# Kernel tuning notes

Measured on AMD Instinct MI355X. Metric: run time of the kernel, lower is better.

The kernel has to match this reference:

```python
import jax, jax.numpy as jnp
import numpy as np

N = 50000        # nodes
E = 800000       # edges (avg degree 16)
D_IN = 128
HID = 128
K = 3


def cheb_edge_weights(row, col, n):
    # PyG ChebConv sym normalization with assumed lambda_max = 2.0:
    # L_hat = (2/lambda_max) * (I - D^-1/2 A D^-1/2) - I = -D^-1/2 A D^-1/2 (zero diagonal)
    mask = (row != col).astype(jnp.float32)  # remove_self_loops
    deg = jax.ops.segment_sum(mask, row, num_segments=n)
    dinv = jnp.where(deg > 0.0, jax.lax.rsqrt(jnp.maximum(deg, 1.0)), 0.0)
    return -dinv[row] * dinv[col] * mask  # [E]


def cheb_conv(x, row, col, w_edge, W, b, n):
    # Chebyshev recursion: Tx0=x, Tx1=L_hat x, Tx_k = 2 L_hat Tx_{k-1} - Tx_{k-2}
    def prop(h):  # sparse L_hat @ h via gather + segment_sum
        return jax.ops.segment_sum(w_edge[:, None] * h[col], row, num_segments=n)

    Tx0 = x
    out = Tx0 @ W[0]
    Tx1 = prop(Tx0)
    out = out + Tx1 @ W[1]
    for k in range(2, W.shape[0]):
        Tx2 = 2.0 * prop(Tx1) - Tx0
        out = out + Tx2 @ W[k]
        Tx0, Tx1 = Tx1, Tx2
    return out + b


def setup_inputs() -> dict:
    key = jax.random.key(0)
    ks = jax.random.split(key, 8)
    x = jax.random.normal(ks[0], (N, D_IN), dtype=jnp.float32)
    ei = jax.random.randint(ks[1], (2, E), 0, N, dtype=jnp.int32)
    s = 0.05
    W1 = jax.random.normal(ks[2], (K, D_IN, HID), dtype=jnp.float32) * s
    b1 = jnp.zeros((HID,), dtype=jnp.float32)
    W2 = jax.random.normal(ks[3], (K, HID, HID), dtype=jnp.float32) * s
    b2 = jnp.zeros((HID,), dtype=jnp.float32)
    W3 = jax.random.normal(ks[4], (K, HID, HID), dtype=jnp.float32) * s
    b3 = jnp.zeros((HID,), dtype=jnp.float32)
    return {"x": x, "ei": ei, "W1": W1, "b1": b1, "W2": W2, "b2": b2, "W3": W3, "b3": b3}


def reference(x, ei, W1, b1, W2, b2, W3, b3):
    row, col = ei[0], ei[1]
    w_edge = cheb_edge_weights(row, col, N)
    # layer chain: ChebConv -> ReLU -> dropout (eval mode: identity)
    h = jax.nn.relu(cheb_conv(x, row, col, w_edge, W1, b1, N))
    h = jax.nn.relu(cheb_conv(h, row, col, w_edge, W2, b2, N))
    h = jax.nn.relu(cheb_conv(h, row, col, w_edge, W3, b3, N))
    return h
```

## Files before the change

kernel.cpp:

```cpp
#include <hip/hip_runtime.h>
#include <hip/hip_bf16.h>

#define DFEAT 128

typedef short bf16x8 __attribute__((ext_vector_type(8)));
typedef float f32x4  __attribute__((ext_vector_type(4)));
typedef unsigned short u16x8 __attribute__((ext_vector_type(8)));

__device__ __forceinline__ unsigned bf16r(float f) {
    unsigned u = __float_as_uint(f);
    u += 0x7fffu + ((u >> 16) & 1u);
    return u >> 16;
}
__device__ __forceinline__ unsigned pack_bf16(float lo, float hi) {
    return bf16r(lo) | (bf16r(hi) << 16);
}

__global__ void deg_kernel(const int* __restrict__ ei, int* __restrict__ deg, int E) {
    int e = blockIdx.x * blockDim.x + threadIdx.x;
    if (e < E) {
        int r = ei[e];
        int c = ei[E + e];
        if (r != c) atomicAdd(&deg[r], 1);
    }
}

__global__ void dinv_kernel(const int* __restrict__ deg, float* __restrict__ dinv, int n) {
    int i = blockIdx.x * blockDim.x + threadIdx.x;
    if (i < n) {
        int d = deg[i];
        dinv[i] = (d > 0) ? rsqrtf((float)d) : 0.f;
    }
}

__global__ __launch_bounds__(1024) void scan1_kernel(const int* __restrict__ deg,
                                                     int* __restrict__ row_ptr,
                                                     int* __restrict__ bsum, int n) {
    __shared__ int wsums[16];
    int t = threadIdx.x;
    int idx = blockIdx.x * 1024 + t;
    int v = (idx < n) ? deg[idx] : 0;
    int vi = v;
    #pragma unroll
    for (int off = 1; off < 64; off <<= 1) {
        int x = __shfl_up(vi, off);
        if ((t & 63) >= off) vi += x;
    }
    if ((t & 63) == 63) wsums[t >> 6] = vi;
    __syncthreads();
    if (t < 16) {
        int s = wsums[t];
        int si = s;
        #pragma unroll
        for (int off = 1; off < 16; off <<= 1) {
            int x = __shfl_up(si, off);
            if (t >= off) si += x;
        }
        wsums[t] = si - s;
        if (t == 15) bsum[blockIdx.x] = si;
    }
    __syncthreads();
    if (idx < n) row_ptr[idx + 1] = wsums[t >> 6] + vi;
}

__global__ void scan2_kernel(int* __restrict__ bsum, int nb) {
    int t = threadIdx.x;
    int carry = 0;
    for (int base = 0; base < nb; base += 64) {
        int v = (base + t < nb) ? bsum[base + t] : 0;
        int vi = v;
        #pragma unroll
        for (int off = 1; off < 64; off <<= 1) {
            int x = __shfl_up(vi, off);
            if (t >= off) vi += x;
        }
        if (base + t < nb) bsum[base + t] = carry + vi - v;
        carry += __shfl(vi, 63);
    }
}

__global__ __launch_bounds__(1024) void scan3_kernel(int* __restrict__ row_ptr,
                                                     const int* __restrict__ bsum, int n) {
    int idx = blockIdx.x * 1024 + threadIdx.x;
    if (idx == 0) row_ptr[0] = 0;
    if (idx < n) row_ptr[idx + 1] += bsum[blockIdx.x];
}

__global__ void fill_kernel(const int* __restrict__ ei, const int* __restrict__ row_ptr,
                            int* __restrict__ fillc, const float* __restrict__ dinv,
                            int* __restrict__ e_col, float* __restrict__ e_w, int E) {
    int e = blockIdx.x * blockDim.x + threadIdx.x;
    if (e < E) {
        int r = ei[e];
        int c = ei[E + e];
        if (r != c) {
            int pos = row_ptr[r] + atomicAdd(&fillc[r], 1);
            e_col[pos] = c;
            e_w[pos] = -dinv[r] * dinv[c];
        }
    }
}

__global__ void xconv_kernel(const float2* __restrict__ x, unsigned* __restrict__ xb, int n2) {
    int id = blockIdx.x * blockDim.x + threadIdx.x;
    if (id < n2) {
        float2 v = x[id];
        xb[id] = pack_bf16(v.x, v.y);
    }
}

__global__ void wprep_kernel(const float* __restrict__ W1, const float* __restrict__ W2,
                             const float* __restrict__ W3, unsigned short* __restrict__ Wt) {
    int id = blockIdx.x * blockDim.x + threadIdx.x;
    const int PER = 3 * DFEAT * DFEAT;
    if (id < 3 * PER) {
        int layer = id / PER;
        int rem = id - layer * PER;
        const float* W = (layer == 0) ? W1 : ((layer == 1) ? W2 : W3);
        int seg = rem >> 14;
        int k   = (rem >> 7) & 127;
        int nn  = rem & 127;
        Wt[layer * PER + (seg << 14) + (nn << 7) + k] = (unsigned short)bf16r(W[rem]);
    }
}

__global__ __launch_bounds__(256) void prop_bf16_kernel(
    const unsigned* __restrict__ hin, const unsigned* __restrict__ sub,
    unsigned* __restrict__ hout,
    const int* __restrict__ row_ptr, const int* __restrict__ e_col,
    const float* __restrict__ e_w, float alpha, int n)
{
    int wv = __builtin_amdgcn_readfirstlane(threadIdx.x >> 6);
    int node = blockIdx.x * 4 + wv;
    int t = threadIdx.x & 63;
    if (node >= n) return;
    int s = row_ptr[node];
    int e = row_ptr[node + 1];
    float a0 = 0.f, a1 = 0.f;
    int j = s;
    for (; j + 8 <= e; j += 8) {
        int c0 = e_col[j+0], c1 = e_col[j+1], c2 = e_col[j+2], c3 = e_col[j+3];
        int c4 = e_col[j+4], c5 = e_col[j+5], c6 = e_col[j+6], c7 = e_col[j+7];
        float w0 = e_w[j+0], w1 = e_w[j+1], w2 = e_w[j+2], w3 = e_w[j+3];
        float w4 = e_w[j+4], w5 = e_w[j+5], w6 = e_w[j+6], w7 = e_w[j+7];
        unsigned v0 = hin[(size_t)c0 * 64 + t];
        unsigned v1 = hin[(size_t)c1 * 64 + t];
        unsigned v2 = hin[(size_t)c2 * 64 + t];
        unsigned v3 = hin[(size_t)c3 * 64 + t];
        unsigned v4 = hin[(size_t)c4 * 64 + t];
        unsigned v5 = hin[(size_t)c5 * 64 + t];
        unsigned v6 = hin[(size_t)c6 * 64 + t];
        unsigned v7 = hin[(size_t)c7 * 64 + t];
        a0 += w0 * __uint_as_float(v0 << 16);  a1 += w0 * __uint_as_float(v0 & 0xffff0000u);
        a0 += w1 * __uint_as_float(v1 << 16);  a1 += w1 * __uint_as_float(v1 & 0xffff0000u);
        a0 += w2 * __uint_as_float(v2 << 16);  a1 += w2 * __uint_as_float(v2 & 0xffff0000u);
        a0 += w3 * __uint_as_float(v3 << 16);  a1 += w3 * __uint_as_float(v3 & 0xffff0000u);
        a0 += w4 * __uint_as_float(v4 << 16);  a1 += w4 * __uint_as_float(v4 & 0xffff0000u);
        a0 += w5 * __uint_as_float(v5 << 16);  a1 += w5 * __uint_as_float(v5 & 0xffff0000u);
        a0 += w6 * __uint_as_float(v6 << 16);  a1 += w6 * __uint_as_float(v6 & 0xffff0000u);
        a0 += w7 * __uint_as_float(v7 << 16);  a1 += w7 * __uint_as_float(v7 & 0xffff0000u);
    }
    for (; j < e; ++j) {
        int c = e_col[j];
        float w = e_w[j];
        unsigned v = hin[(size_t)c * 64 + t];
        a0 += w * __uint_as_float(v << 16);
        a1 += w * __uint_as_float(v & 0xffff0000u);
    }
    a0 *= alpha; a1 *= alpha;
    if (sub) {
        unsigned v = sub[(size_t)node * 64 + t];
        a0 -= __uint_as_float(v << 16);
        a1 -= __uint_as_float(v & 0xffff0000u);
    }
    hout[(size_t)node * 64 + t] = pack_bf16(a0, a1);
}

#define WPAD 136
__global__ __launch_bounds__(256) void gemm3_mfma_kernel(
    const unsigned short* __restrict__ X0, const unsigned short* __restrict__ X1,
    const unsigned short* __restrict__ X2,
    const unsigned short* __restrict__ Wt, const float* __restrict__ bias,
    void* __restrict__ out, int n, int out_bf16)
{
    __shared__ unsigned short Ws[DFEAT * WPAD];
    const int t    = threadIdx.x;
    const int wave = t >> 6;
    const int lane = t & 63;
    const int quad = lane >> 4;
    const int l16  = lane & 15;

    const int row_base = blockIdx.x * 128 + wave * 32;
    int r0 = row_base + l16;       if (r0 >= n) r0 = n - 1;
    int r1 = row_base + 16 + l16;  if (r1 >= n) r1 = n - 1;

    const unsigned short* Xps[3] = {X0, X1, X2};

    f32x4 acc[2][8];
    #pragma unroll
    for (int tt = 0; tt < 2; ++tt)
        #pragma unroll
        for (int c = 0; c < 8; ++c) acc[tt][c] = (f32x4){0.f, 0.f, 0.f, 0.f};

    const int srow = t >> 1;
    const int shalf = (t & 1) * 64;

    #pragma unroll
    for (int seg = 0; seg < 3; ++seg) {
        __syncthreads();
        const unsigned short* Wp = Wt + (seg << 14);
        #pragma unroll
        for (int i = 0; i < 8; ++i) {
            *(u16x8*)&Ws[srow * WPAD + shalf + i * 8] =
                *(const u16x8*)&Wp[srow * DFEAT + shalf + i * 8];
        }
        __syncthreads();
        const unsigned short* A0 = Xps[seg] + (size_t)r0 * DFEAT;
        const unsigned short* A1 = Xps[seg] + (size_t)r1 * DFEAT;
        #pragma unroll
        for (int kk = 0; kk < 4; ++kk) {
            const int ko = kk * 32 + quad * 8;
            bf16x8 a0 = *(const bf16x8*)(A0 + ko);
            bf16x8 a1 = *(const bf16x8*)(A1 + ko);
            #pragma unroll
            for (int c = 0; c < 8; ++c) {
                bf16x8 b = *(const bf16x8*)&Ws[(c * 16 + l16) * WPAD + ko];
                acc[0][c] = __builtin_amdgcn_mfma_f32_16x16x32_bf16(a0, b, acc[0][c], 0, 0, 0);
                acc[1][c] = __builtin_amdgcn_mfma_f32_16x16x32_bf16(a1, b, acc[1][c], 0, 0, 0);
            }
        }
    }

    #pragma unroll
    for (int tt = 0; tt < 2; ++tt) {
        int orow0 = blockIdx.x * 128 + wave * 32 + tt * 16 + quad * 4;
        #pragma unroll
        for (int c = 0; c < 8; ++c) {
            int col = c * 16 + l16;
            float bv = bias[col];
            #pragma unroll
            for (int r = 0; r < 4; ++r) {
                int orow = orow0 + r;
                if (orow < n) {
                    float v = fmaxf(acc[tt][c][r] + bv, 0.f);
                    if (out_bf16)
                        ((unsigned short*)out)[(size_t)orow * DFEAT + col] = (unsigned short)bf16r(v);
                    else
                        ((float*)out)[(size_t)orow * DFEAT + col] = v;
                }
            }
        }
    }
}

extern "C" void kernel_launch(void* const* d_in, const int* in_sizes, int n_in,
                              void* d_out, int out_size, void* d_ws, size_t ws_size,
                              hipStream_t stream) {
    const float* x  = (const float*)d_in[0];
    const int*   ei = (const int*)d_in[1];
    const float* W1 = (const float*)d_in[2];
    const float* b1 = (const float*)d_in[3];
    const float* W2 = (const float*)d_in[4];
    const float* b2 = (const float*)d_in[5];
    const float* W3 = (const float*)d_in[6];
    const float* b3 = (const float*)d_in[7];

    const int N = in_sizes[0] / DFEAT;
    const int E = in_sizes[1] / 2;
    const int NPK = N * (DFEAT / 2);
    const int NB = (N + 1023) / 1024;

    unsigned* xb  = (unsigned*)d_ws;
    unsigned* t1b = xb  + NPK;
    unsigned* t2b = t1b + NPK;
    unsigned* ab  = t2b + NPK;
    unsigned short* wt = (unsigned short*)(ab + NPK);
    int*   deg     = (int*)(wt + 3 * 3 * DFEAT * DFEAT);
    int*   fillc   = deg + N;
    int*   row_ptr = fillc + N;
    float* dinv    = (float*)(row_ptr + (N + 1));
    int*   e_col   = (int*)(dinv + N);
    float* e_w     = (float*)(e_col + E);
    int*   bsum    = (int*)(e_w + E);

    hipMemsetAsync(deg,   0, sizeof(int) * N, stream);
    hipMemsetAsync(fillc, 0, sizeof(int) * N, stream);

    deg_kernel<<<(E + 255) / 256, 256, 0, stream>>>(ei, deg, E);
    scan1_kernel<<<NB, 1024, 0, stream>>>(deg, row_ptr, bsum, N);
    scan2_kernel<<<1, 64, 0, stream>>>(bsum, NB);
    scan3_kernel<<<NB, 1024, 0, stream>>>(row_ptr, bsum, N);
    dinv_kernel<<<(N + 255) / 256, 256, 0, stream>>>(deg, dinv, N);
    fill_kernel<<<(E + 255) / 256, 256, 0, stream>>>(ei, row_ptr, fillc, dinv, e_col, e_w, E);

    xconv_kernel<<<(NPK + 255) / 256, 256, 0, stream>>>((const float2*)x, xb, NPK);
    const int WELEM = 3 * DFEAT * DFEAT;
    wprep_kernel<<<(3 * WELEM + 255) / 256, 256, 0, stream>>>(W1, W2, W3, wt);

    const float* bl[3] = {b1, b2, b3};
    const unsigned* hin = xb;
    const int prop_grid = (N + 3) / 4;
    const int gemm_grid = (N + 127) / 128;
    for (int l = 0; l < 3; ++l) {
        prop_bf16_kernel<<<prop_grid, 256, 0, stream>>>(hin, nullptr, t1b, row_ptr, e_col, e_w, 1.f, N);
        prop_bf16_kernel<<<prop_grid, 256, 0, stream>>>(t1b, hin, t2b, row_ptr, e_col, e_w, 2.f, N);
        void* hout = (l == 2) ? d_out : (void*)ab;
        gemm3_mfma_kernel<<<gemm_grid, 256, 0, stream>>>(
            (const unsigned short*)hin, (const unsigned short*)t1b, (const unsigned short*)t2b,
            wt + l * WELEM, bl[l], hout, N, (l == 2) ? 0 : 1);
        hin = ab;
    }
}
```

Baseline: 435.2 us.

## Pack edge column and fp16 weight into one word, privatize CSR build counters

```diff
diff --git a/kernel.cpp b/kernel.cpp
--- a/kernel.cpp
+++ b/kernel.cpp
@@ -16,31 +16,36 @@
     return bf16r(lo) | (bf16r(hi) << 16);
 }
 
-__global__ void deg_kernel(const int* __restrict__ ei, int* __restrict__ deg, int E) {
+__global__ void deg_kernel(const int* __restrict__ ei, int* __restrict__ deg8, int E, int N) {
     int e = blockIdx.x * blockDim.x + threadIdx.x;
     if (e < E) {
         int r = ei[e];
         int c = ei[E + e];
-        if (r != c) atomicAdd(&deg[r], 1);
-    }
-}
-
-__global__ void dinv_kernel(const int* __restrict__ deg, float* __restrict__ dinv, int n) {
-    int i = blockIdx.x * blockDim.x + threadIdx.x;
-    if (i < n) {
-        int d = deg[i];
-        dinv[i] = (d > 0) ? rsqrtf((float)d) : 0.f;
-    }
-}
-
-__global__ __launch_bounds__(1024) void scan1_kernel(const int* __restrict__ deg,
+        if (r != c) atomicAdd(&deg8[(blockIdx.x & 7) * N + r], 1);
+    }
+}
+
+__global__ __launch_bounds__(1024) void scan1_kernel(const int* __restrict__ deg8,
+                                                     int* __restrict__ poff,
                                                      int* __restrict__ row_ptr,
-                                                     int* __restrict__ bsum, int n) {
+                                                     int* __restrict__ bsum,
+                                                     float* __restrict__ dinv, int n) {
     __shared__ int wsums[16];
     int t = threadIdx.x;
     int idx = blockIdx.x * 1024 + t;
-    int v = (idx < n) ? deg[idx] : 0;
-    int vi = v;
+    int tot = 0;
+    if (idx < n) {
+        int run = 0;
+        #pragma unroll
+        for (int p = 0; p < 8; ++p) {
+            int d = deg8[p * n + idx];
+            poff[p * n + idx] = run;
+            run += d;
+        }
+        tot = run;
+        dinv[idx] = (tot > 0) ? rsqrtf((float)tot) : 0.f;
+    }
+    int vi = tot;
     #pragma unroll
     for (int off = 1; off < 64; off <<= 1) {
         int x = __shfl_up(vi, off);
@@ -87,16 +92,22 @@
 }
 
 __global__ void fill_kernel(const int* __restrict__ ei, const int* __restrict__ row_ptr,
-                            int* __restrict__ fillc, const float* __restrict__ dinv,
-                            int* __restrict__ e_col, float* __restrict__ e_w, int E) {
+                            const int* __restrict__ poff, int* __restrict__ fillc8,
+                            const float* __restrict__ dinv,
+                            unsigned* __restrict__ e_cw, int E, int N) {
     int e = blockIdx.x * blockDim.x + threadIdx.x;
     if (e < E) {
         int r = ei[e];
         int c = ei[E + e];
         if (r != c) {
-            int pos = row_ptr[r] + atomicAdd(&fillc[r], 1);
-            e_col[pos] = c;
-            e_w[pos] = -dinv[r] * dinv[c];
+            int p = blockIdx.x & 7;
+            int k = atomicAdd(&fillc8[p * N + r], 1);
+            int pos = row_ptr[r] + poff[p * N + r] + k;
+            float w = -dinv[r] * dinv[c];
+            _Float16 hf = (_Float16)w;
+            unsigned short wb;
+            __builtin_memcpy(&wb, &hf, 2);
+            e_cw[pos] = (unsigned)c | ((unsigned)wb << 16);
         }
     }
 }
@@ -127,8 +138,8 @@
 __global__ __launch_bounds__(256) void prop_bf16_kernel(
     const unsigned* __restrict__ hin, const unsigned* __restrict__ sub,
     unsigned* __restrict__ hout,
-    const int* __restrict__ row_ptr, const int* __restrict__ e_col,
-    const float* __restrict__ e_w, float alpha, int n)
+    const int* __restrict__ row_ptr, const unsigned* __restrict__ e_cw,
+    float alpha, int n)
 {
     int wv = __builtin_amdgcn_readfirstlane(threadIdx.x >> 6);
     int node = blockIdx.x * 4 + wv;
@@ -138,32 +149,46 @@
     int e = row_ptr[node + 1];
     float a0 = 0.f, a1 = 0.f;
     int j = s;
-    for (; j + 8 <= e; j += 8) {
-        int c0 = e_col[j+0], c1 = e_col[j+1], c2 = e_col[j+2], c3 = e_col[j+3];
-        int c4 = e_col[j+4], c5 = e_col[j+5], c6 = e_col[j+6], c7 = e_col[j+7];
-        float w0 = e_w[j+0], w1 = e_w[j+1], w2 = e_w[j+2], w3 = e_w[j+3];
-        float w4 = e_w[j+4], w5 = e_w[j+5], w6 = e_w[j+6], w7 = e_w[j+7];
-        unsigned v0 = hin[(size_t)c0 * 64 + t];
-        unsigned v1 = hin[(size_t)c1 * 64 + t];
-        unsigned v2 = hin[(size_t)c2 * 64 + t];
-        unsigned v3 = hin[(size_t)c3 * 64 + t];
-        unsigned v4 = hin[(size_t)c4 * 64 + t];
-        unsigned v5 = hin[(size_t)c5 * 64 + t];
-        unsigned v6 = hin[(size_t)c6 * 64 + t];
-        unsigned v7 = hin[(size_t)c7 * 64 + t];
-        a0 += w0 * __uint_as_float(v0 << 16);  a1 += w0 * __uint_as_float(v0 & 0xffff0000u);
-        a0 += w1 * __uint_as_float(v1 << 16);  a1 += w1 * __uint_as_float(v1 & 0xffff0000u);
-        a0 += w2 * __uint_as_float(v2 << 16);  a1 += w2 * __uint_as_float(v2 & 0xffff0000u);
-        a0 += w3 * __uint_as_float(v3 << 16);  a1 += w3 * __uint_as_float(v3 & 0xffff0000u);
-        a0 += w4 * __uint_as_float(v4 << 16);  a1 += w4 * __uint_as_float(v4 & 0xffff0000u);
-        a0 += w5 * __uint_as_float(v5 << 16);  a1 += w5 * __uint_as_float(v5 & 0xffff0000u);
-        a0 += w6 * __uint_as_float(v6 << 16);  a1 += w6 * __uint_as_float(v6 & 0xffff0000u);
-        a0 += w7 * __uint_as_float(v7 << 16);  a1 += w7 * __uint_as_float(v7 & 0xffff0000u);
+    for (; j + 16 <= e; j += 16) {
+        unsigned cw[16];
+        #pragma unroll
+        for (int q = 0; q < 16; ++q) cw[q] = e_cw[j + q];
+        unsigned v[16];
+        #pragma unroll
+        for (int q = 0; q < 16; ++q)
+            v[q] = hin[(size_t)(cw[q] & 0xffffu) * 64 + t];
+        #pragma unroll
+        for (int q = 0; q < 16; ++q) {
+            unsigned short wb = (unsigned short)(cw[q] >> 16);
+            _Float16 hf; __builtin_memcpy(&hf, &wb, 2);
+            float w = (float)hf;
+            a0 += w * __uint_as_float(v[q] << 16);
+            a1 += w * __uint_as_float(v[q] & 0xffff0000u);
+        }
+    }
+    for (; j + 4 <= e; j += 4) {
+        unsigned cw[4];
+        #pragma unroll
+        for (int q = 0; q < 4; ++q) cw[q] = e_cw[j + q];
+        unsigned v[4];
+        #pragma unroll
+        for (int q = 0; q < 4; ++q)
+            v[q] = hin[(size_t)(cw[q] & 0xffffu) * 64 + t];
+        #pragma unroll
+        for (int q = 0; q < 4; ++q) {
+            unsigned short wb = (unsigned short)(cw[q] >> 16);
+            _Float16 hf; __builtin_memcpy(&hf, &wb, 2);
+            float w = (float)hf;
+            a0 += w * __uint_as_float(v[q] << 16);
+            a1 += w * __uint_as_float(v[q] & 0xffff0000u);
+        }
     }
     for (; j < e; ++j) {
-        int c = e_col[j];
-        float w = e_w[j];
-        unsigned v = hin[(size_t)c * 64 + t];
+        unsigned cwv = e_cw[j];
+        unsigned short wb = (unsigned short)(cwv >> 16);
+        _Float16 hf; __builtin_memcpy(&hf, &wb, 2);
+        float w = (float)hf;
+        unsigned v = hin[(size_t)(cwv & 0xffffu) * 64 + t];
         a0 += w * __uint_as_float(v << 16);
         a1 += w * __uint_as_float(v & 0xffff0000u);
     }
@@ -275,23 +300,22 @@
     unsigned* t2b = t1b + NPK;
     unsigned* ab  = t2b + NPK;
     unsigned short* wt = (unsigned short*)(ab + NPK);
-    int*   deg     = (int*)(wt + 3 * 3 * DFEAT * DFEAT);
-    int*   fillc   = deg + N;
-    int*   row_ptr = fillc + N;
+    int*   deg8    = (int*)(wt + 3 * 3 * DFEAT * DFEAT);
+    int*   poff    = deg8 + 8 * N;
+    int*   fillc8  = poff + 8 * N;
+    int*   row_ptr = fillc8 + 8 * N;
     float* dinv    = (float*)(row_ptr + (N + 1));
-    int*   e_col   = (int*)(dinv + N);
-    float* e_w     = (float*)(e_col + E);
-    int*   bsum    = (int*)(e_w + E);
-
-    hipMemsetAsync(deg,   0, sizeof(int) * N, stream);
-    hipMemsetAsync(fillc, 0, sizeof(int) * N, stream);
-
-    deg_kernel<<<(E + 255) / 256, 256, 0, stream>>>(ei, deg, E);
-    scan1_kernel<<<NB, 1024, 0, stream>>>(deg, row_ptr, bsum, N);
+    unsigned* e_cw = (unsigned*)(dinv + N);
+    int*   bsum    = (int*)(e_cw + E);
+
+    hipMemsetAsync(deg8,   0, sizeof(int) * 8 * N, stream);
+    hipMemsetAsync(fillc8, 0, sizeof(int) * 8 * N, stream);
+
+    deg_kernel<<<(E + 255) / 256, 256, 0, stream>>>(ei, deg8, E, N);
+    scan1_kernel<<<NB, 1024, 0, stream>>>(deg8, poff, row_ptr, bsum, dinv, N);
     scan2_kernel<<<1, 64, 0, stream>>>(bsum, NB);
     scan3_kernel<<<NB, 1024, 0, stream>>>(row_ptr, bsum, N);
-    dinv_kernel<<<(N + 255) / 256, 256, 0, stream>>>(deg, dinv, N);
-    fill_kernel<<<(E + 255) / 256, 256, 0, stream>>>(ei, row_ptr, fillc, dinv, e_col, e_w, E);
+    fill_kernel<<<(E + 255) / 256, 256, 0, stream>>>(ei, row_ptr, poff, fillc8, dinv, e_cw, E, N);
 
     xconv_kernel<<<(NPK + 255) / 256, 256, 0, stream>>>((const float2*)x, xb, NPK);
     const int WELEM = 3 * DFEAT * DFEAT;
@@ -302,8 +326,8 @@
     const int prop_grid = (N + 3) / 4;
     const int gemm_grid = (N + 127) / 128;
     for (int l = 0; l < 3; ++l) {
-        prop_bf16_kernel<<<prop_grid, 256, 0, stream>>>(hin, nullptr, t1b, row_ptr, e_col, e_w, 1.f, N);
-        prop_bf16_kernel<<<prop_grid, 256, 0, stream>>>(t1b, hin, t2b, row_ptr, e_col, e_w, 2.f, N);
+        prop_bf16_kernel<<<prop_grid, 256, 0, stream>>>(hin, nullptr, t1b, row_ptr, e_cw, 1.f, N);
+        prop_bf16_kernel<<<prop_grid, 256, 0, stream>>>(t1b, hin, t2b, row_ptr, e_cw, 2.f, N);
         void* hout = (l == 2) ? d_out : (void*)ab;
         gemm3_mfma_kernel<<<gemm_grid, 256, 0, stream>>>(
             (const unsigned short*)hin, (const unsigned short*)t1b, (const unsigned short*)t2b,
```

Result: faster. 409.5 us (-5.9%).
